# Optimization experiments

Measured on AMD Instinct MI355X. Metric: run time of the kernel, lower is better.

The kernel has to match this reference:

```python
import jax, jax.numpy as jnp
import numpy as np

N_NODES = 50000
N_EDGES = 1600000
HIDDEN = 256
N_GRAPHS = 1024
N_PROPS = 8
N_FEAT = 4
IN_DIM = N_FEAT + 4 * 8 + 4 * 8  # 68


def setup_inputs() -> dict:
    key = jax.random.key(0)
    ks = jax.random.split(key, 20)
    s = 0.05
    inp = {
        "x": jax.random.randint(ks[0], (N_NODES, N_FEAT), 0, 720),
        "edge_index": jax.random.randint(ks[1], (2, N_EDGES), 0, N_NODES),
        "batch": jnp.sort(jax.random.randint(ks[2], (N_NODES,), 0, N_GRAPHS)),
        "emb24": jax.random.normal(ks[3], (24, 8), jnp.float32) * s,
        "emb72": jax.random.normal(ks[4], (72, 8), jnp.float32) * s,
        "lin1_w": jax.random.normal(ks[5], (HIDDEN, IN_DIM), jnp.float32) * s,
        "lin1_b": jnp.zeros((HIDDEN,), jnp.float32),
        "qa1_w": jax.random.normal(ks[6], (HIDDEN, HIDDEN), jnp.float32) * s,
        "qa1_b": jnp.zeros((HIDDEN,), jnp.float32),
        "lin2_w": jax.random.normal(ks[7], (HIDDEN, HIDDEN), jnp.float32) * s,
        "lin2_b": jnp.zeros((HIDDEN,), jnp.float32),
        "qa2_w": jax.random.normal(ks[8], (HIDDEN, HIDDEN), jnp.float32) * s,
        "qa2_b": jnp.zeros((HIDDEN,), jnp.float32),
        "head_w1": jax.random.normal(ks[9], (N_PROPS, HIDDEN // 2, HIDDEN), jnp.float32) * s,
        "head_b1": jnp.zeros((N_PROPS, HIDDEN // 2), jnp.float32),
        "head_w2": jax.random.normal(ks[10], (N_PROPS, 1, HIDDEN // 2), jnp.float32) * s,
        "head_b2": jnp.zeros((N_PROPS, 1), jnp.float32),
    }
    return inp


def _qagcn_conv(h, src, dst, lin_w, lin_b, qa_w, qa_b):
    n = h.shape[0]
    lin_x = h @ lin_w.T + lin_b                                  # [N, H]
    # message = lin(x_j); aggr='add' over edges; add_self_loops contributes
    # one extra lin_x per node, and update() adds lin(x) again -> 2*lin_x.
    aggr = jax.ops.segment_sum(lin_x[src], dst, num_segments=n)  # [N, H]
    h2 = aggr + 2.0 * lin_x
    b, e, _, _ = jnp.split(h2, 4, axis=-1)
    h3 = jnp.concatenate([b, e, b + e, b + 2.0 * e], axis=-1)
    return jax.nn.relu(h3 @ qa_w.T + qa_b)


def reference(x, edge_index, batch, emb24, emb72, lin1_w, lin1_b, qa1_w, qa1_b,
              lin2_w, lin2_b, qa2_w, qa2_b, head_w1, head_b1, head_w2, head_b2):
    n = x.shape[0]
    r24 = emb24[x % 24].reshape(n, -1)          # [N, 32]
    r72 = emb72[x % 72].reshape(n, -1)          # [N, 32]
    h = jnp.concatenate([x.astype(jnp.float32), r24, r72], axis=-1)  # [N, 68]
    src, dst = edge_index[0], edge_index[1]
    h = _qagcn_conv(h, src, dst, lin1_w, lin1_b, qa1_w, qa1_b)
    h = _qagcn_conv(h, src, dst, lin2_w, lin2_b, qa2_w, qa2_b)
    # global mean pool over graphs
    sums = jax.ops.segment_sum(h, batch, num_segments=N_GRAPHS)      # [G, H]
    cnts = jax.ops.segment_sum(jnp.ones((n,), h.dtype), batch, num_segments=N_GRAPHS)
    g = sums / jnp.maximum(cnts, 1.0)[:, None]                       # [G, H]
    # per-property 2-layer MLP heads
    h1 = jax.nn.relu(jnp.einsum('gd,phd->pgh', g, head_w1) + head_b1[:, None, :])
    out = jnp.einsum('pgh,poh->pgo', h1, head_w2) + head_b2[:, None, :]  # [P, G, 1]
    return out[..., 0].T                                             # [G, P]
```

## Files before the change

### kernel.cpp

```cpp
#include <hip/hip_runtime.h>
#include <hip/hip_bf16.h>

#define N_NODESC 50000
#define N_EDGESC 1600000
#define NGC 1024
#define NPC 8
#define NBIN 196
#define NBLKE 391

typedef __attribute__((ext_vector_type(8))) short bf16x8;
typedef __attribute__((ext_vector_type(4))) float f32x4;

__device__ inline ushort f2bf(float f) {
  union { float f; uint u; } v; v.f = f;
  uint u = v.u;
  u += 0x7FFF + ((u >> 16) & 1);
  return (ushort)(u >> 16);
}
__device__ inline float bflo(uint u) {
  union { uint u; float f; } v; v.u = u << 16; return v.f;
}
__device__ inline float bfhi(uint u) {
  union { uint u; float f; } v; v.u = u & 0xFFFF0000u; return v.f;
}

__global__ __launch_bounds__(256) void megaprep(
    const float* __restrict__ qa1w, const float* __restrict__ qa2w,
    const float* __restrict__ lin1w, const float* __restrict__ lin2w,
    ushort* __restrict__ qe1, ushort* __restrict__ qe2,
    ushort* __restrict__ l1w, ushort* __restrict__ l2w,
    const int* __restrict__ x, const float* __restrict__ e24,
    const float* __restrict__ e72, ushort* __restrict__ feat,
    const int* __restrict__ dst, int* __restrict__ bh) {
  int bid = blockIdx.x, t = threadIdx.x;
  if (bid < 256) {
    const float* qw = (bid < 128) ? qa1w : qa2w;
    ushort* eff = (bid < 128) ? qe1 : qe2;
    int k = (bid & 127) * 2 + (t >> 7);
    int j = t & 127;
    const float* r = qw + (size_t)k * 256;
    float v;
    if (j < 64) v = r[j] + r[128 + j] + r[192 + j];
    else { int j2 = j - 64; v = r[64 + j2] + r[128 + j2] + 2.0f * r[192 + j2]; }
    eff[(size_t)k * 128 + j] = f2bf(v);
  } else if (bid < 304) {
    int i = (bid - 256) * 256 + t;
    int r = i / 96, c = i - r * 96;
    l1w[i] = (c < 68) ? f2bf(lin1w[(size_t)r * 68 + c]) : (ushort)0;
  } else if (bid < 432) {
    int r = bid - 304;
    l2w[(size_t)r * 256 + t] = f2bf(lin2w[(size_t)r * 256 + t]);
  } else if (bid < 1456) {
    const int stride = 1024 * 256;
    for (int i = (bid - 432) * 256 + t; i < N_NODESC * 96; i += stride) {
      int n = i / 96, tt = i - n * 96;
      float v = 0.f;
      if (tt < 4) v = (float)x[n * 4 + tt];
      else if (tt < 36) { int kk = tt - 4;  int f = kk >> 3, c = kk & 7; v = e24[(x[n * 4 + f] % 24) * 8 + c]; }
      else if (tt < 68) { int kk = tt - 36; int f = kk >> 3, c = kk & 7; v = e72[(x[n * 4 + f] % 72) * 8 + c]; }
      feat[i] = f2bf(v);
    }
  } else {
    __shared__ int hist[NBIN];
    int blk = bid - 1456;
    if (t < NBIN) hist[t] = 0;
    __syncthreads();
    int base = blk * 4096;
#pragma unroll
    for (int i = 0; i < 16; ++i) {
      int idx = base + i * 256 + t;
      if (idx < N_EDGESC) atomicAdd(&hist[dst[idx] >> 8], 1);
    }
    __syncthreads();
    if (t < NBIN) bh[(size_t)t * NBLKE + blk] = hist[t];
  }
}

__global__ __launch_bounds__(64) void csr_scan_bins(int* __restrict__ bh, int* __restrict__ bt) {
  int bin = blockIdx.x;
  int lane = threadIdx.x;
  int carry = 0;
  int* row = bh + (size_t)bin * NBLKE;
  for (int c = 0; c < NBLKE; c += 64) {
    int j = c + lane;
    int v = (j < NBLKE) ? row[j] : 0;
    int incl = v;
#pragma unroll
    for (int off = 1; off < 64; off <<= 1) {
      int u = __shfl_up(incl, off, 64);
      if (lane >= off) incl += u;
    }
    if (j < NBLKE) row[j] = carry + incl - v;
    carry += __shfl(incl, 63, 64);
  }
  if (lane == 0) bt[bin] = carry;
}

__global__ __launch_bounds__(256) void csr_scatter(const int* __restrict__ src,
                                                   const int* __restrict__ dst,
                                                   const int* __restrict__ bh,
                                                   const int* __restrict__ bt,
                                                   uint* __restrict__ tmp, int E) {
  __shared__ int sc[256];
  __shared__ int cur[NBIN];
  int t = threadIdx.x, blk = blockIdx.x;
  int v = (t < NBIN) ? bt[t] : 0;
  sc[t] = v;
  __syncthreads();
  for (int off = 1; off < 256; off <<= 1) {
    int u = (t >= off) ? sc[t - off] : 0;
    __syncthreads();
    sc[t] += u;
    __syncthreads();
  }
  if (t < NBIN) cur[t] = (sc[t] - v) + bh[(size_t)t * NBLKE + blk];
  __syncthreads();
  int base = blk * 4096;
#pragma unroll
  for (int i = 0; i < 16; ++i) {
    int idx = base + i * 256 + t;
    if (idx < E) {
      int d = dst[idx];
      uint p = ((uint)d << 16) | (uint)src[idx];
      int pos = atomicAdd(&cur[d >> 8], 1);
      tmp[pos] = p;
    }
  }
}

__global__ __launch_bounds__(256) void csr_bucket_sort(const uint* __restrict__ tmp,
                                                       const int* __restrict__ bt,
                                                       ushort* __restrict__ elist,
                                                       int* __restrict__ rp) {
  __shared__ int sc[256];
  __shared__ int cnt[256];
  int b = blockIdx.x, t = threadIdx.x;
  int v = (t < NBIN) ? bt[t] : 0;
  sc[t] = v;
  __syncthreads();
  for (int off = 1; off < 256; off <<= 1) {
    int u = (t >= off) ? sc[t - off] : 0;
    __syncthreads();
    sc[t] += u;
    __syncthreads();
  }
  int base = (b == 0) ? 0 : sc[b - 1];
  int end = sc[b];
  int total = sc[NBIN - 1];
  __syncthreads();
  cnt[t] = 0;
  __syncthreads();
  for (int i = base + t; i < end; i += 256)
    atomicAdd(&cnt[(tmp[i] >> 16) & 255], 1);
  __syncthreads();
  int cv = cnt[t];
  sc[t] = cv;
  __syncthreads();
  for (int off = 1; off < 256; off <<= 1) {
    int u = (t >= off) ? sc[t - off] : 0;
    __syncthreads();
    sc[t] += u;
    __syncthreads();
  }
  int excl = sc[t] - cv;
  int node = (b << 8) + t;
  if (node < N_NODESC) rp[node] = base + excl;
  if (b == NBIN - 1 && t == 0) rp[N_NODESC] = total;
  cnt[t] = base + excl;
  __syncthreads();
  for (int i = base + t; i < end; i += 256) {
    uint p = tmp[i];
    int pos = atomicAdd(&cnt[(p >> 16) & 255], 1);
    elist[pos] = (ushort)(p & 0xFFFFu);
  }
}

template <int K>
__global__ __launch_bounds__(256, 2) void mfma_gemm_lds(
    const ushort* __restrict__ A, const ushort* __restrict__ W,
    const float* __restrict__ bias, ushort* __restrict__ C,
    int M, int NC, int relu) {
  __shared__ ushort ws[128 * K];
  int tid = threadIdx.x;
  int lane = tid & 63;
  int wv = tid >> 6;
  int rbase = blockIdx.x * 128 + wv * 32;
  int colt = blockIdx.y * 128;
  int r16 = lane & 15;
  int kg = (lane >> 4) * 8;

  const char* wt = (const char*)(W + (size_t)colt * K);
#pragma unroll
  for (int i = 0; i < K / 16; ++i) {
    int o = (i * 256 + tid) * 16;
    int col = o / (2 * K);
    int sw = o ^ ((col & 7) << 4);
    *(bf16x8*)((char*)ws + sw) = *(const bf16x8*)(wt + o);
  }
  __syncthreads();

  f32x4 acc[2][8];
#pragma unroll
  for (int m = 0; m < 2; ++m)
#pragma unroll
    for (int n = 0; n < 8; ++n) acc[m][n] = (f32x4){0.f, 0.f, 0.f, 0.f};

  for (int k0 = 0; k0 < K; k0 += 32) {
    bf16x8 a[2], b[8];
#pragma unroll
    for (int m = 0; m < 2; ++m) {
      int rr = rbase + m * 16 + r16;
      if (rr >= M) rr = M - 1;
      a[m] = *(const bf16x8*)(A + (size_t)rr * K + k0 + kg);
    }
#pragma unroll
    for (int n = 0; n < 8; ++n) {
      int cl = n * 16 + r16;
      int byte = (cl * 2 * K + (k0 + kg) * 2) ^ ((cl & 7) << 4);
      b[n] = *(const bf16x8*)((const char*)ws + byte);
    }
#pragma unroll
    for (int m = 0; m < 2; ++m)
#pragma unroll
      for (int n = 0; n < 8; ++n)
        acc[m][n] = __builtin_amdgcn_mfma_f32_16x16x32_bf16(a[m], b[n], acc[m][n], 0, 0, 0);
  }

  int rowoff = (lane >> 4) * 4;
#pragma unroll
  for (int m = 0; m < 2; ++m) {
#pragma unroll
    for (int j = 0; j < 4; ++j) {
      int row = rbase + m * 16 + rowoff + j;
      if (row >= M) continue;
#pragma unroll
      for (int n = 0; n < 8; ++n) {
        int col = colt + n * 16 + r16;
        float v = acc[m][n][j] + bias[col];
        if (relu) v = fmaxf(v, 0.f);
        C[(size_t)row * NC + col] = f2bf(v);
      }
    }
  }
}

__global__ __launch_bounds__(256) void aggregate2(const uint* __restrict__ lx,
                                                  const int* __restrict__ rp,
                                                  const ushort* __restrict__ elist,
                                                  uint* __restrict__ h2) {
  int wv = threadIdx.x >> 6, lane = threadIdx.x & 63;
  int n = blockIdx.x * 4 + wv;
  int beg = rp[n], end = rp[n + 1];
  uint u = lx[(size_t)n * 64 + lane];
  float a0 = 2.f * bflo(u), a1 = 2.f * bfhi(u);
  int e = beg;
  for (; e + 8 <= end; e += 8) {
    int s0 = elist[e], s1 = elist[e + 1], s2 = elist[e + 2], s3 = elist[e + 3];
    int s4 = elist[e + 4], s5 = elist[e + 5], s6 = elist[e + 6], s7 = elist[e + 7];
    uint u0 = lx[(size_t)s0 * 64 + lane];
    uint u1 = lx[(size_t)s1 * 64 + lane];
    uint u2 = lx[(size_t)s2 * 64 + lane];
    uint u3 = lx[(size_t)s3 * 64 + lane];
    uint u4 = lx[(size_t)s4 * 64 + lane];
    uint u5 = lx[(size_t)s5 * 64 + lane];
    uint u6 = lx[(size_t)s6 * 64 + lane];
    uint u7 = lx[(size_t)s7 * 64 + lane];
    a0 += bflo(u0) + bflo(u1) + bflo(u2) + bflo(u3);
    a1 += bfhi(u0) + bfhi(u1) + bfhi(u2) + bfhi(u3);
    a0 += bflo(u4) + bflo(u5) + bflo(u6) + bflo(u7);
    a1 += bfhi(u4) + bfhi(u5) + bfhi(u6) + bfhi(u7);
  }
  for (; e < end; ++e) {
    uint u0 = lx[(size_t)elist[e] * 64 + lane];
    a0 += bflo(u0);
    a1 += bfhi(u0);
  }
  h2[(size_t)n * 64 + lane] = (uint)f2bf(a0) | ((uint)f2bf(a1) << 16);
}

__global__ __launch_bounds__(128) void pool2(const uint* __restrict__ h,
                                             const int* __restrict__ batch,
                                             float* __restrict__ g) {
  int gg = blockIdx.x;
  int j = threadIdx.x;
  int lo = 0, hi = N_NODESC;
  while (lo < hi) { int mid = (lo + hi) >> 1; if (batch[mid] < gg) lo = mid + 1; else hi = mid; }
  int beg = lo;
  hi = N_NODESC;
  while (lo < hi) { int mid = (lo + hi) >> 1; if (batch[mid] < gg + 1) lo = mid + 1; else hi = mid; }
  int end = lo;
  float a0 = 0.f, a1 = 0.f;
  for (int n = beg; n < end; ++n) {
    uint u = h[(size_t)n * 128 + j];
    a0 += bflo(u);
    a1 += bfhi(u);
  }
  float c = fmaxf((float)(end - beg), 1.0f);
  g[(size_t)gg * 256 + 2 * j] = a0 / c;
  g[(size_t)gg * 256 + 2 * j + 1] = a1 / c;
}

__global__ __launch_bounds__(128) void head_kernel(const float* __restrict__ g,
    const float* __restrict__ w1, const float* __restrict__ b1,
    const float* __restrict__ w2, const float* __restrict__ b2,
    float* __restrict__ out) {
  int p = blockIdx.y;
  int g0 = blockIdx.x * 8;
  int t = threadIdx.x;
  __shared__ float gs[8][256];
  for (int i = t; i < 8 * 256; i += 128)
    gs[i >> 8][i & 255] = g[(size_t)(g0 + (i >> 8)) * 256 + (i & 255)];
  __syncthreads();
  const float4* w4 = (const float4*)(w1 + ((size_t)p * 128 + t) * 256);
  float bv = b1[p * 128 + t];
  float acc[8];
#pragma unroll
  for (int q = 0; q < 8; ++q) acc[q] = bv;
  for (int d4 = 0; d4 < 64; ++d4) {
    float4 wv = w4[d4];
#pragma unroll
    for (int q = 0; q < 8; ++q) {
      acc[q] += gs[q][d4 * 4 + 0] * wv.x + gs[q][d4 * 4 + 1] * wv.y +
                gs[q][d4 * 4 + 2] * wv.z + gs[q][d4 * 4 + 3] * wv.w;
    }
  }
  float w2v = w2[p * 128 + t];
  __shared__ float red[2][8];
  int wave = t >> 6, lane = t & 63;
#pragma unroll
  for (int q = 0; q < 8; ++q) {
    float v = fmaxf(acc[q], 0.f) * w2v;
    for (int o = 32; o > 0; o >>= 1) v += __shfl_down(v, o, 64);
    if (lane == 0) red[wave][q] = v;
  }
  __syncthreads();
  if (t < 8) out[(size_t)(g0 + t) * 8 + p] = red[0][t] + red[1][t] + b2[p];
}

extern "C" void kernel_launch(void* const* d_in, const int* in_sizes, int n_in,
                              void* d_out, int out_size, void* d_ws, size_t ws_size,
                              hipStream_t stream) {
  const int*   x     = (const int*)d_in[0];
  const int*   ei    = (const int*)d_in[1];
  const int*   batch = (const int*)d_in[2];
  const float* emb24 = (const float*)d_in[3];
  const float* emb72 = (const float*)d_in[4];
  const float* lin1w = (const float*)d_in[5];
  const float* lin1b = (const float*)d_in[6];
  const float* qa1w  = (const float*)d_in[7];
  const float* qa1b  = (const float*)d_in[8];
  const float* lin2w = (const float*)d_in[9];
  const float* lin2b = (const float*)d_in[10];
  const float* qa2w  = (const float*)d_in[11];
  const float* qa2b  = (const float*)d_in[12];
  const float* hw1   = (const float*)d_in[13];
  const float* hb1   = (const float*)d_in[14];
  const float* hw2   = (const float*)d_in[15];
  const float* hb2   = (const float*)d_in[16];
  float* out = (float*)d_out;

  const int* srcv = ei;
  const int* dstv = ei + N_EDGESC;

  char* wsb = (char*)d_ws;
  size_t off = 0;
  auto alloc = [&](size_t b) { char* p = wsb + off; off += (b + 255) & ~(size_t)255; return p; };
  ushort* feat  = (ushort*)alloc((size_t)N_NODESC * 96 * 2);
  ushort* linx  = (ushort*)alloc((size_t)N_NODESC * 128 * 2);
  ushort* h2    = (ushort*)alloc((size_t)N_NODESC * 128 * 2);
  ushort* h     = (ushort*)alloc((size_t)N_NODESC * 256 * 2);
  float*  gbuf  = (float*)alloc((size_t)NGC * 256 * 4);
  ushort* qe1   = (ushort*)alloc(256 * 128 * 2);
  ushort* qe2   = (ushort*)alloc(256 * 128 * 2);
  ushort* l1w   = (ushort*)alloc(128 * 96 * 2);
  ushort* l2w   = (ushort*)alloc(128 * 256 * 2);
  int*    rp    = (int*)alloc((size_t)(N_NODESC + 1) * 4);
  ushort* elist = (ushort*)alloc((size_t)N_EDGESC * 2);
  int*    bh    = (int*)alloc((size_t)NBIN * NBLKE * 4);
  int*    bt    = (int*)alloc((size_t)NBIN * 4);
  uint*   tmp   = (uint*)h;

  megaprep<<<1847, 256, 0, stream>>>(qa1w, qa2w, lin1w, lin2w, qe1, qe2, l1w, l2w,
                                     x, emb24, emb72, feat, dstv, bh);

  csr_scan_bins<<<NBIN, 64, 0, stream>>>(bh, bt);
  csr_scatter<<<NBLKE, 256, 0, stream>>>(srcv, dstv, bh, bt, tmp, N_EDGESC);
  csr_bucket_sort<<<NBIN, 256, 0, stream>>>(tmp, bt, elist, rp);

  int gm = (N_NODESC + 127) / 128;

  mfma_gemm_lds<96><<<dim3(gm, 1), 256, 0, stream>>>(feat, l1w, lin1b, linx, N_NODESC, 128, 0);
  aggregate2<<<N_NODESC / 4, 256, 0, stream>>>((const uint*)linx, rp, elist, (uint*)h2);
  mfma_gemm_lds<128><<<dim3(gm, 2), 256, 0, stream>>>(h2, qe1, qa1b, h, N_NODESC, 256, 1);

  mfma_gemm_lds<256><<<dim3(gm, 1), 256, 0, stream>>>(h, l2w, lin2b, linx, N_NODESC, 128, 0);
  aggregate2<<<N_NODESC / 4, 256, 0, stream>>>((const uint*)linx, rp, elist, (uint*)h2);
  mfma_gemm_lds<128><<<dim3(gm, 2), 256, 0, stream>>>(h2, qe2, qa2b, h, N_NODESC, 256, 1);

  pool2<<<NGC, 128, 0, stream>>>((const uint*)h, batch, gbuf);
  head_kernel<<<dim3(NGC / 8, NPC), 128, 0, stream>>>(gbuf, hw1, hb1, hw2, hb2, out);
}
```

Baseline: 270.3 us.

## Split lin output into column halves, fuse scatter with lin1, widen pool

The lin1/lin2 GEMM outputs are now stored as two 64-column planes, each N×64 bf16. The aggregation runs one pass per plane, so each gather pass touches a smaller table that fits cache better, and two half-waves walk alternating edges before a shuffle reduction. The CSR scatter and the lin1 GEMM are merged into one launch by block-id dispatch so they overlap. The pooling kernel uses 256 threads that split the rows. Costs are extra index math, more aggregation blocks, and GEMM A/C addressing tied to the split layout.

Result: slower. 288.7 us (+6.8%).

```diff
diff --git a/kernel.cpp b/kernel.cpp
--- a/kernel.cpp
+++ b/kernel.cpp
@@ -96,35 +96,122 @@
   if (lane == 0) bt[bin] = carry;
 }
 
-__global__ __launch_bounds__(256) void csr_scatter(const int* __restrict__ src,
-                                                   const int* __restrict__ dst,
-                                                   const int* __restrict__ bh,
-                                                   const int* __restrict__ bt,
-                                                   uint* __restrict__ tmp, int E) {
-  __shared__ int sc[256];
-  __shared__ int cur[NBIN];
-  int t = threadIdx.x, blk = blockIdx.x;
-  int v = (t < NBIN) ? bt[t] : 0;
-  sc[t] = v;
-  __syncthreads();
-  for (int off = 1; off < 256; off <<= 1) {
-    int u = (t >= off) ? sc[t - off] : 0;
-    __syncthreads();
-    sc[t] += u;
-    __syncthreads();
-  }
-  if (t < NBIN) cur[t] = (sc[t] - v) + bh[(size_t)t * NBLKE + blk];
-  __syncthreads();
-  int base = blk * 4096;
-#pragma unroll
-  for (int i = 0; i < 16; ++i) {
-    int idx = base + i * 256 + t;
-    if (idx < E) {
-      int d = dst[idx];
-      uint p = ((uint)d << 16) | (uint)src[idx];
-      int pos = atomicAdd(&cur[d >> 8], 1);
-      tmp[pos] = p;
-    }
+template <int K, int ASPLIT, int CSPLIT>
+__device__ __forceinline__ void gemm_body(ushort* ws, int bx, int by,
+    const ushort* __restrict__ A, const ushort* __restrict__ W,
+    const float* __restrict__ bias, ushort* __restrict__ C,
+    int M, int NC, int relu) {
+  int tid = threadIdx.x;
+  int lane = tid & 63;
+  int wv = tid >> 6;
+  int rbase = bx * 128 + wv * 32;
+  int colt = by * 128;
+  int r16 = lane & 15;
+  int kg = (lane >> 4) * 8;
+
+  const char* wt = (const char*)(W + (size_t)colt * K);
+#pragma unroll
+  for (int i = 0; i < K / 16; ++i) {
+    int o = (i * 256 + tid) * 16;
+    int col = o / (2 * K);
+    int sw = o ^ ((col & 7) << 4);
+    *(bf16x8*)((char*)ws + sw) = *(const bf16x8*)(wt + o);
+  }
+  __syncthreads();
+
+  f32x4 acc[2][8];
+#pragma unroll
+  for (int m = 0; m < 2; ++m)
+#pragma unroll
+    for (int n = 0; n < 8; ++n) acc[m][n] = (f32x4){0.f, 0.f, 0.f, 0.f};
+
+  for (int k0 = 0; k0 < K; k0 += 32) {
+    int ks = k0 + kg;
+    bf16x8 a[2], b[8];
+#pragma unroll
+    for (int m = 0; m < 2; ++m) {
+      int rr = rbase + m * 16 + r16;
+      if (rr >= M) rr = M - 1;
+      const ushort* ap = ASPLIT ? (A + ((size_t)(ks >> 6) * N_NODESC + rr) * 64 + (ks & 63))
+                                : (A + (size_t)rr * K + ks);
+      a[m] = *(const bf16x8*)ap;
+    }
+#pragma unroll
+    for (int n = 0; n < 8; ++n) {
+      int cl = n * 16 + r16;
+      int byte = (cl * 2 * K + ks * 2) ^ ((cl & 7) << 4);
+      b[n] = *(const bf16x8*)((const char*)ws + byte);
+    }
+#pragma unroll
+    for (int m = 0; m < 2; ++m)
+#pragma unroll
+      for (int n = 0; n < 8; ++n)
+        acc[m][n] = __builtin_amdgcn_mfma_f32_16x16x32_bf16(a[m], b[n], acc[m][n], 0, 0, 0);
+  }
+
+  int rowoff = (lane >> 4) * 4;
+#pragma unroll
+  for (int m = 0; m < 2; ++m) {
+#pragma unroll
+    for (int j = 0; j < 4; ++j) {
+      int row = rbase + m * 16 + rowoff + j;
+      if (row >= M) continue;
+#pragma unroll
+      for (int n = 0; n < 8; ++n) {
+        int col = colt + n * 16 + r16;
+        float v = acc[m][n][j] + bias[col];
+        if (relu) v = fmaxf(v, 0.f);
+        size_t idx = CSPLIT ? ((size_t)(col >> 6) * N_NODESC + row) * 64 + (col & 63)
+                            : (size_t)row * NC + col;
+        C[idx] = f2bf(v);
+      }
+    }
+  }
+}
+
+template <int K, int ASPLIT, int CSPLIT>
+__global__ __launch_bounds__(256, 2) void mfma_gemm_lds(
+    const ushort* __restrict__ A, const ushort* __restrict__ W,
+    const float* __restrict__ bias, ushort* __restrict__ C,
+    int M, int NC, int relu) {
+  __shared__ ushort ws[128 * K];
+  gemm_body<K, ASPLIT, CSPLIT>(ws, blockIdx.x, blockIdx.y, A, W, bias, C, M, NC, relu);
+}
+
+__global__ __launch_bounds__(256, 2) void scatter_lin1(
+    const int* __restrict__ src, const int* __restrict__ dst,
+    const int* __restrict__ bh, const int* __restrict__ bt, uint* __restrict__ tmp,
+    const ushort* __restrict__ feat, const ushort* __restrict__ l1w,
+    const float* __restrict__ lin1b, ushort* __restrict__ linx) {
+  __shared__ ushort ws[128 * 96];
+  int bid = blockIdx.x, t = threadIdx.x;
+  if (bid < NBLKE) {
+    int* sc = (int*)ws;
+    int* cur = sc + 256;
+    int v = (t < NBIN) ? bt[t] : 0;
+    sc[t] = v;
+    __syncthreads();
+    for (int off = 1; off < 256; off <<= 1) {
+      int u = (t >= off) ? sc[t - off] : 0;
+      __syncthreads();
+      sc[t] += u;
+      __syncthreads();
+    }
+    if (t < NBIN) cur[t] = (sc[t] - v) + bh[(size_t)t * NBLKE + bid];
+    __syncthreads();
+    int base = bid * 4096;
+#pragma unroll
+    for (int i = 0; i < 16; ++i) {
+      int idx = base + i * 256 + t;
+      if (idx < N_EDGESC) {
+        int d = dst[idx];
+        uint p = ((uint)d << 16) | (uint)src[idx];
+        int pos = atomicAdd(&cur[d >> 8], 1);
+        tmp[pos] = p;
+      }
+    }
+  } else {
+    gemm_body<96, 0, 1>(ws, bid - NBLKE, 0, feat, l1w, lin1b, linx, N_NODESC, 128, 0);
   }
 }
 
@@ -175,114 +262,58 @@
   }
 }
 
-template <int K>
-__global__ __launch_bounds__(256, 2) void mfma_gemm_lds(
-    const ushort* __restrict__ A, const ushort* __restrict__ W,
-    const float* __restrict__ bias, ushort* __restrict__ C,
-    int M, int NC, int relu) {
-  __shared__ ushort ws[128 * K];
-  int tid = threadIdx.x;
-  int lane = tid & 63;
-  int wv = tid >> 6;
-  int rbase = blockIdx.x * 128 + wv * 32;
-  int colt = blockIdx.y * 128;
-  int r16 = lane & 15;
-  int kg = (lane >> 4) * 8;
-
-  const char* wt = (const char*)(W + (size_t)colt * K);
-#pragma unroll
-  for (int i = 0; i < K / 16; ++i) {
-    int o = (i * 256 + tid) * 16;
-    int col = o / (2 * K);
-    int sw = o ^ ((col & 7) << 4);
-    *(bf16x8*)((char*)ws + sw) = *(const bf16x8*)(wt + o);
-  }
-  __syncthreads();
-
-  f32x4 acc[2][8];
-#pragma unroll
-  for (int m = 0; m < 2; ++m)
-#pragma unroll
-    for (int n = 0; n < 8; ++n) acc[m][n] = (f32x4){0.f, 0.f, 0.f, 0.f};
-
-  for (int k0 = 0; k0 < K; k0 += 32) {
-    bf16x8 a[2], b[8];
-#pragma unroll
-    for (int m = 0; m < 2; ++m) {
-      int rr = rbase + m * 16 + r16;
-      if (rr >= M) rr = M - 1;
-      a[m] = *(const bf16x8*)(A + (size_t)rr * K + k0 + kg);
-    }
-#pragma unroll
-    for (int n = 0; n < 8; ++n) {
-      int cl = n * 16 + r16;
-      int byte = (cl * 2 * K + (k0 + kg) * 2) ^ ((cl & 7) << 4);
-      b[n] = *(const bf16x8*)((const char*)ws + byte);
-    }
-#pragma unroll
-    for (int m = 0; m < 2; ++m)
-#pragma unroll
-      for (int n = 0; n < 8; ++n)
-        acc[m][n] = __builtin_amdgcn_mfma_f32_16x16x32_bf16(a[m], b[n], acc[m][n], 0, 0, 0);
-  }
-
-  int rowoff = (lane >> 4) * 4;
-#pragma unroll
-  for (int m = 0; m < 2; ++m) {
-#pragma unroll
-    for (int j = 0; j < 4; ++j) {
-      int row = rbase + m * 16 + rowoff + j;
-      if (row >= M) continue;
-#pragma unroll
-      for (int n = 0; n < 8; ++n) {
-        int col = colt + n * 16 + r16;
-        float v = acc[m][n][j] + bias[col];
-        if (relu) v = fmaxf(v, 0.f);
-        C[(size_t)row * NC + col] = f2bf(v);
-      }
-    }
-  }
-}
-
-__global__ __launch_bounds__(256) void aggregate2(const uint* __restrict__ lx,
-                                                  const int* __restrict__ rp,
-                                                  const ushort* __restrict__ elist,
-                                                  uint* __restrict__ h2) {
+__global__ __launch_bounds__(256) void aggregate_h(const uint* __restrict__ lx,
+                                                   const int* __restrict__ rp,
+                                                   const ushort* __restrict__ elist,
+                                                   uint* __restrict__ h2) {
+  const int BPP = N_NODESC / 4;
+  int bid = blockIdx.x;
+  int pass = bid / BPP;
+  int nb = bid - pass * BPP;
+  const uint* T = lx + (size_t)pass * N_NODESC * 32;
+  uint* O = h2 + (size_t)pass * N_NODESC * 32;
   int wv = threadIdx.x >> 6, lane = threadIdx.x & 63;
-  int n = blockIdx.x * 4 + wv;
+  int half = lane >> 5, c = lane & 31;
+  int n = nb * 4 + wv;
   int beg = rp[n], end = rp[n + 1];
-  uint u = lx[(size_t)n * 64 + lane];
-  float a0 = 2.f * bflo(u), a1 = 2.f * bfhi(u);
-  int e = beg;
-  for (; e + 8 <= end; e += 8) {
-    int s0 = elist[e], s1 = elist[e + 1], s2 = elist[e + 2], s3 = elist[e + 3];
-    int s4 = elist[e + 4], s5 = elist[e + 5], s6 = elist[e + 6], s7 = elist[e + 7];
-    uint u0 = lx[(size_t)s0 * 64 + lane];
-    uint u1 = lx[(size_t)s1 * 64 + lane];
-    uint u2 = lx[(size_t)s2 * 64 + lane];
-    uint u3 = lx[(size_t)s3 * 64 + lane];
-    uint u4 = lx[(size_t)s4 * 64 + lane];
-    uint u5 = lx[(size_t)s5 * 64 + lane];
-    uint u6 = lx[(size_t)s6 * 64 + lane];
-    uint u7 = lx[(size_t)s7 * 64 + lane];
+  float a0 = 0.f, a1 = 0.f;
+  int e = beg + half;
+  for (; e + 14 < end; e += 16) {
+    int s0 = elist[e], s1 = elist[e + 2], s2 = elist[e + 4], s3 = elist[e + 6];
+    int s4 = elist[e + 8], s5 = elist[e + 10], s6 = elist[e + 12], s7 = elist[e + 14];
+    uint u0 = T[(size_t)s0 * 32 + c];
+    uint u1 = T[(size_t)s1 * 32 + c];
+    uint u2 = T[(size_t)s2 * 32 + c];
+    uint u3 = T[(size_t)s3 * 32 + c];
+    uint u4 = T[(size_t)s4 * 32 + c];
+    uint u5 = T[(size_t)s5 * 32 + c];
+    uint u6 = T[(size_t)s6 * 32 + c];
+    uint u7 = T[(size_t)s7 * 32 + c];
     a0 += bflo(u0) + bflo(u1) + bflo(u2) + bflo(u3);
     a1 += bfhi(u0) + bfhi(u1) + bfhi(u2) + bfhi(u3);
     a0 += bflo(u4) + bflo(u5) + bflo(u6) + bflo(u7);
     a1 += bfhi(u4) + bfhi(u5) + bfhi(u6) + bfhi(u7);
   }
-  for (; e < end; ++e) {
-    uint u0 = lx[(size_t)elist[e] * 64 + lane];
-    a0 += bflo(u0);
-    a1 += bfhi(u0);
-  }
-  h2[(size_t)n * 64 + lane] = (uint)f2bf(a0) | ((uint)f2bf(a1) << 16);
-}
-
-__global__ __launch_bounds__(128) void pool2(const uint* __restrict__ h,
+  for (; e < end; e += 2) {
+    uint u = T[(size_t)elist[e] * 32 + c];
+    a0 += bflo(u);
+    a1 += bfhi(u);
+  }
+  a0 += __shfl_xor(a0, 32);
+  a1 += __shfl_xor(a1, 32);
+  if (half == 0) {
+    uint su = T[(size_t)n * 32 + c];
+    O[(size_t)n * 32 + c] = (uint)f2bf(a0 + 2.f * bflo(su)) |
+                            ((uint)f2bf(a1 + 2.f * bfhi(su)) << 16);
+  }
+}
+
+__global__ __launch_bounds__(256) void pool2(const uint* __restrict__ h,
                                              const int* __restrict__ batch,
                                              float* __restrict__ g) {
   int gg = blockIdx.x;
-  int j = threadIdx.x;
+  int t = threadIdx.x;
+  int j = t & 127, rg = t >> 7;
   int lo = 0, hi = N_NODESC;
   while (lo < hi) { int mid = (lo + hi) >> 1; if (batch[mid] < gg) lo = mid + 1; else hi = mid; }
   int beg = lo;
@@ -290,14 +321,28 @@
   while (lo < hi) { int mid = (lo + hi) >> 1; if (batch[mid] < gg + 1) lo = mid + 1; else hi = mid; }
   int end = lo;
   float a0 = 0.f, a1 = 0.f;
-  for (int n = beg; n < end; ++n) {
+  int n = beg + rg;
+  for (; n + 2 < end; n += 4) {
+    uint u = h[(size_t)n * 128 + j];
+    uint u2 = h[(size_t)(n + 2) * 128 + j];
+    a0 += bflo(u) + bflo(u2);
+    a1 += bfhi(u) + bfhi(u2);
+  }
+  if (n < end) {
     uint u = h[(size_t)n * 128 + j];
     a0 += bflo(u);
     a1 += bfhi(u);
   }
-  float c = fmaxf((float)(end - beg), 1.0f);
-  g[(size_t)gg * 256 + 2 * j] = a0 / c;
-  g[(size_t)gg * 256 + 2 * j + 1] = a1 / c;
+  __shared__ float s0[128], s1[128];
+  if (rg == 1) { s0[j] = a0; s1[j] = a1; }
+  __syncthreads();
+  if (rg == 0) {
+    a0 += s0[j];
+    a1 += s1[j];
+    float cfac = fmaxf((float)(end - beg), 1.0f);
+    g[(size_t)gg * 256 + 2 * j] = a0 / cfac;
+    g[(size_t)gg * 256 + 2 * j + 1] = a1 / cfac;
+  }
 }
 
 __global__ __launch_bounds__(128) void head_kernel(const float* __restrict__ g,
@@ -382,21 +427,21 @@
 
   megaprep<<<1847, 256, 0, stream>>>(qa1w, qa2w, lin1w, lin2w, qe1, qe2, l1w, l2w,
                                      x, emb24, emb72, feat, dstv, bh);
-
   csr_scan_bins<<<NBIN, 64, 0, stream>>>(bh, bt);
-  csr_scatter<<<NBLKE, 256, 0, stream>>>(srcv, dstv, bh, bt, tmp, N_EDGESC);
+
+  int gm = (N_NODESC + 127) / 128;
+
+  scatter_lin1<<<NBLKE + gm, 256, 0, stream>>>(srcv, dstv, bh, bt, tmp,
+                                               feat, l1w, lin1b, linx);
   csr_bucket_sort<<<NBIN, 256, 0, stream>>>(tmp, bt, elist, rp);
 
-  int gm = (N_NODESC + 127) / 128;
-
-  mfma_gemm_lds<96><<<dim3(gm, 1), 256, 0, stream>>>(feat, l1w, lin1b, linx, N_NODESC, 128, 0);
-  aggregate2<<<N_NODESC / 4, 256, 0, stream>>>((const uint*)linx, rp, elist, (uint*)h2);
-  mfma_gemm_lds<128><<<dim3(gm, 2), 256, 0, stream>>>(h2, qe1, qa1b, h, N_NODESC, 256, 1);
-
-  mfma_gemm_lds<256><<<dim3(gm, 1), 256, 0, stream>>>(h, l2w, lin2b, linx, N_NODESC, 128, 0);
-  aggregate2<<<N_NODESC / 4, 256, 0, stream>>>((const uint*)linx, rp, elist, (uint*)h2);
-  mfma_gemm_lds<128><<<dim3(gm, 2), 256, 0, stream>>>(h2, qe2, qa2b, h, N_NODESC, 256, 1);
-
-  pool2<<<NGC, 128, 0, stream>>>((const uint*)h, batch, gbuf);
+  aggregate_h<<<(N_NODESC / 4) * 2, 256, 0, stream>>>((const uint*)linx, rp, elist, (uint*)h2);
+  mfma_gemm_lds<128, 1, 0><<<dim3(gm, 2), 256, 0, stream>>>(h2, qe1, qa1b, h, N_NODESC, 256, 1);
+
+  mfma_gemm_lds<256, 0, 1><<<dim3(gm, 1), 256, 0, stream>>>(h, l2w, lin2b, linx, N_NODESC, 128, 0);
+  aggregate_h<<<(N_NODESC / 4) * 2, 256, 0, stream>>>((const uint*)linx, rp, elist, (uint*)h2);
+  mfma_gemm_lds<128, 1, 0><<<dim3(gm, 2), 256, 0, stream>>>(h2, qe2, qa2b, h, N_NODESC, 256, 1);
+
+  pool2<<<NGC, 256, 0, stream>>>((const uint*)h, batch, gbuf);
   head_kernel<<<dim3(NGC / 8, NPC), 128, 0, stream>>>(gbuf, hw1, hb1, hw2, hb2, out);
 }
```
